# Performance work log

Measured on AMD Instinct MI355X. Metric: run time of the kernel, lower is better.

The kernel has to match this reference:

```python
import jax, jax.numpy as jnp
import numpy as np
from jax import lax

# Static config (matches init_kwargs)
DIM = 256; DR = 4; GROUP = 2; NH = 4; KS = 3; NA = 1; NUM_CLASS = 80; MUL = 5.0
CR = DIM // DR            # reduced dim = 64
GC = CR // GROUP          # offset-group channels = 32
HC = CR // NH             # per-head dim = 16
SCALE = HC ** -0.5
B, H, W = 8, 64, 64


def setup_inputs() -> dict:
    key = jax.random.key(0)
    ks_ = jax.random.split(key, 8)
    x = jax.random.normal(ks_[0], (B, DIM, H, W), jnp.float32)
    # offset = absolute pixel coordinates of the base sampling grid
    offset = jax.random.uniform(ks_[1], (B, NA * 2 * KS * KS, H, W), jnp.float32) * (H - 1)
    return dict(
        x=x, offset=offset,
        ln1_g=jnp.ones((DIM,), jnp.float32), ln1_b=jnp.zeros((DIM,), jnp.float32),
        w_qkv=jax.random.normal(ks_[2], (3 * CR, DIM), jnp.float32) * 0.02,
        w_dw=jax.random.normal(ks_[3], (GC, 1, 3, 3), jnp.float32) * 0.1,
        ln2_g=jnp.ones((GC,), jnp.float32), ln2_b=jnp.zeros((GC,), jnp.float32),
        w_off=jax.random.normal(ks_[4], (NA * 2 * KS * KS, GC, 3, 3), jnp.float32) * 0.02,
        b_off=jnp.zeros((NA * 2 * KS * KS,), jnp.float32),
        rpb_table=jax.random.normal(ks_[5], (1, NH, 1, 1, KS * KS, HC), jnp.float32) * 0.02,
        w_proj=jax.random.normal(ks_[6], (DIM, CR), jnp.float32) * 0.02,
        b_proj=jnp.zeros((DIM,), jnp.float32),
        w_cls=jax.random.normal(ks_[7], (NUM_CLASS, DIM), jnp.float32) * 0.02,
        b_cls=jnp.zeros((NUM_CLASS,), jnp.float32),
    )


def _ln_chw(x, g, b, eps=1e-5):
    # LayerNorm over channel dim of NCHW tensor (LayerNormProxy)
    xt = jnp.moveaxis(x, 1, -1)
    m = xt.mean(-1, keepdims=True)
    v = ((xt - m) ** 2).mean(-1, keepdims=True)
    y = (xt - m) * lax.rsqrt(v + eps) * g + b
    return jnp.moveaxis(y, -1, 1)


def _conv(x, w, groups=1, pad=1):
    return lax.conv_general_dilated(x, w, (1, 1), [(pad, pad), (pad, pad)],
                                    feature_group_count=groups,
                                    dimension_numbers=('NCHW', 'OIHW', 'NCHW'))


def _grid_sample(img, grid):
    # img [N,C,H,W]; grid [N,Ho,Wo,2] with (x,y) in [-1,1]; bilinear, zeros pad, align_corners=True
    N, C, Hi, Wi = img.shape
    gx = (grid[..., 0] + 1.0) * 0.5 * (Wi - 1)
    gy = (grid[..., 1] + 1.0) * 0.5 * (Hi - 1)
    x0 = jnp.floor(gx); y0 = jnp.floor(gy)
    x1 = x0 + 1.0;      y1 = y0 + 1.0

    def gather(ix, iy):
        valid = (ix >= 0) & (ix <= Wi - 1) & (iy >= 0) & (iy <= Hi - 1)
        ixc = jnp.clip(ix, 0, Wi - 1).astype(jnp.int32)
        iyc = jnp.clip(iy, 0, Hi - 1).astype(jnp.int32)
        v = jax.vmap(lambda im, yy, xx: im[:, yy, xx])(img, iyc, ixc)  # [N,C,Ho,Wo]
        return v * valid[:, None].astype(img.dtype)

    wa = ((x1 - gx) * (y1 - gy))[:, None]
    wb = ((gx - x0) * (y1 - gy))[:, None]
    wc = ((x1 - gx) * (gy - y0))[:, None]
    wd = ((gx - x0) * (gy - y0))[:, None]
    return (gather(x0, y0) * wa + gather(x1, y0) * wb +
            gather(x0, y1) * wc + gather(x1, y1) * wd)


def _extract_feats(feat, off, Hh, Ww):
    # feat [Bg,GC,H,W]; off [Bg, NA*2*KS*KS, H, W] in pixel coords (row, col)
    Bg = feat.shape[0]
    o = off.reshape(Bg, NA, KS, KS, 2, Hh, Ww)
    o = o.transpose(0, 1, 2, 5, 3, 6, 4)                  # b na kh h kw w d
    o = o.reshape(Bg, NA * KS * Hh, KS * Ww, 2)
    gy = 2.0 * o[..., 0] / (Hh - 1) - 1.0                  # row coord
    gx = 2.0 * o[..., 1] / (Ww - 1) - 1.0                  # col coord
    grid = jnp.stack([gx, gy], -1)                         # flip(-1): (x, y)
    out = _grid_sample(feat, grid)                         # [Bg,GC,NA*KS*H,KS*W]
    out = out.reshape(Bg, GC, NA, KS, Hh, KS, Ww)
    out = out.transpose(0, 2, 3, 5, 1, 4, 6).reshape(Bg, NA * KS * KS, GC, Hh, Ww)
    return out


def reference(x, offset, ln1_g, ln1_b, w_qkv, w_dw, ln2_g, ln2_b, w_off, b_off,
              rpb_table, w_proj, b_proj, w_cls, b_cls):
    Bb, C, Hh, Ww = x.shape
    N = KS * KS

    x_ = _ln_chw(x, ln1_g, ln1_b)
    qkv = jnp.einsum('oc,bchw->bohw', w_qkv, x_)           # [B,3*CR,H,W]
    q, k, v = jnp.split(qkv, 3, axis=1)                    # each [B,CR,H,W]

    # --- offset prediction ---
    q_off = q.reshape(Bb * GROUP, GC, Hh, Ww)
    t = _conv(q_off, w_dw, groups=GC)                      # depthwise 3x3
    t = _ln_chw(t, ln2_g, ln2_b)
    t = jax.nn.gelu(t, approximate=False)
    pred_offset = _conv(t, w_off) + b_off[None, :, None, None]

    off = jnp.broadcast_to(offset[:, None], (Bb, GROUP, NA * 2 * N, Hh, Ww))
    off = off.reshape(Bb * GROUP, NA * 2 * N, Hh, Ww)
    off = jnp.tanh(pred_offset) * MUL + off

    # --- deformable gather of k/v ---
    k = _extract_feats(k.reshape(Bb * GROUP, GC, Hh, Ww), off, Hh, Ww)
    v = _extract_feats(v.reshape(Bb * GROUP, GC, Hh, Ww), off, Hh, Ww)

    def to_heads(t):
        # [(b g), na*n, gc, h, w] -> [b, nh, hw, na, n, hc]
        t = t.reshape(Bb, GROUP, NA, N, GC, Hh, Ww)
        t = t.transpose(0, 5, 6, 2, 3, 1, 4)               # b h w na n g gc
        t = t.reshape(Bb, Hh * Ww, NA, N, NH, HC)
        return t.transpose(0, 4, 1, 2, 3, 5)

    k = to_heads(k) + rpb_table                            # [B,NH,HW,NA,N,HC]
    v = to_heads(v)

    q = q.reshape(Bb, NH, HC, Hh * Ww).transpose(0, 1, 3, 2)  # [B,NH,HW,HC]
    q = jnp.broadcast_to((q * SCALE)[:, :, :, None, :], (Bb, NH, Hh * Ww, NA, HC))

    attn = jnp.einsum('bnpac,bnpakc->bnpak', q, k)         # [B,NH,HW,NA,N]
    attn = jax.nn.softmax(attn, axis=-1)
    out = jnp.einsum('bnpak,bnpakc->bnpac', attn, v)       # [B,NH,HW,NA,HC]

    out = out.transpose(0, 2, 3, 1, 4).reshape(Bb, Hh * Ww, NA, CR)
    out = out @ w_proj.T + b_proj                          # [B,HW,NA,C]
    out = out + x.transpose(0, 2, 3, 1).reshape(Bb, Hh * Ww, 1, C)

    cls = out @ w_cls.T + b_cls                            # [B,HW,NA,NUM_CLASS]
    cls = cls.reshape(Bb, Hh, Ww, NA, NUM_CLASS).transpose(0, 3, 4, 1, 2)
    return cls.reshape(Bb, NA * NUM_CLASS, Hh, Ww)
```

## Files before the change

### kernel.cpp

```cpp
#include <hip/hip_runtime.h>
#include <hip/hip_fp16.h>
#include <math.h>

#define BB   8
#define HW   4096
#define BHW  32768
#define DIM  256
#define CR   64
#define GC   32
#define NHD  4
#define HC   16
#define NTAP 9
#define NCLS 80

#define OFF_QP   0u
#define OFF_QT   2097152u
#define OFF_KT   4194304u
#define OFF_T    8388608u
#define OFF_WBF  8388608u
#define OFF_AB   8437760u
#define OFF_OFFB 10485760u
#define OFF_AOT  11665408u
#define OFF_WPT  13762560u
#define OFF_WCT  13778944u
#define OFF_WFT  13799424u

typedef short bf16x8 __attribute__((ext_vector_type(8)));
typedef float f32x4  __attribute__((ext_vector_type(4)));

__device__ __forceinline__ unsigned short f2bf(float f) {
    unsigned u = __float_as_uint(f);
    unsigned r = u + 0x7FFFu + ((u >> 16) & 1u);
    return (unsigned short)(r >> 16);
}

__global__ __launch_bounds__(256) void k0_prep(
    const float* __restrict__ wqkv, const float* __restrict__ g1,
    const float* __restrict__ b1, const float* __restrict__ woff,
    const float* __restrict__ wproj, const float* __restrict__ wcls,
    float* __restrict__ ws)
{
    const int t = threadIdx.x;
    const int blk = blockIdx.x;
    if (blk < 192) {
        const int o = blk;
        unsigned short* wbf = (unsigned short*)(ws + OFF_WBF);
        wbf[o * 256 + t] = f2bf(wqkv[o * 256 + t] * g1[t]);
    } else if (blk < 448) {
        const int r = blk - 192;
        unsigned short* wpb = (unsigned short*)(ws + OFF_WPT);
        unsigned short* wcb = (unsigned short*)(ws + OFF_WCT);
        if (t < 64) wpb[r * 64 + t] = f2bf(wproj[r * 64 + t]);
        if (r < 80) wcb[r * 256 + t] = f2bf(wcls[r * 256 + t]);
    } else {
        if (t < 192) {
            float a = 0.f, bb = 0.f;
            for (int c = 0; c < 256; ++c) {
                float w = wqkv[t * 256 + c];
                a += w * g1[c]; bb += w * b1[c];
            }
            ws[OFF_AB + t] = a;
            ws[OFF_AB + 192 + t] = bb;
            for (int pair = t; pair < 288; pair += 192) {
                int wo = pair >> 5, ic = pair & 31;
                for (int o = 0; o < 18; ++o)
                    ws[OFF_WFT + (wo * 32 + ic) * 18 + o] = woff[(o * 32 + ic) * 9 + wo];
            }
        }
    }
}

__global__ __launch_bounds__(512) void k1_mfma(
    const float* __restrict__ x, float* __restrict__ ws)
{
    __shared__ float tile[64 * 193];
    const int t = threadIdx.x;
    const int b = blockIdx.x & 7, row = blockIdx.x >> 3;
    const int wv = __builtin_amdgcn_readfirstlane(t >> 6);
    const int pt = wv & 3, oh = wv >> 2;
    const int lane = t & 63;
    const int quad = lane >> 4, pxl = lane & 15;
    const int colbase = row * 64 + pt * 16 + pxl;
    const unsigned short* wbf = (const unsigned short*)(ws + OFF_WBF);
    const float* AB = ws + OFF_AB;

    f32x4 acc[6];
    #pragma unroll
    for (int ot = 0; ot < 6; ++ot) acc[ot] = (f32x4){0.f, 0.f, 0.f, 0.f};
    float s = 0.f, ss = 0.f;
    const size_t xb0 = (size_t)b * DIM * HW + colbase;

    for (int ks = 0; ks < 8; ++ks) {
        const int cbase = ks * 32 + quad * 8;
        float xv[8];
        #pragma unroll
        for (int j = 0; j < 8; ++j) {
            xv[j] = x[xb0 + (size_t)(cbase + j) * HW];
            s += xv[j]; ss += xv[j] * xv[j];
        }
        union { bf16x8 v; unsigned short u[8]; } bfrag;
        #pragma unroll
        for (int j = 0; j < 8; ++j) bfrag.u[j] = f2bf(xv[j]);
        #pragma unroll
        for (int ot = 0; ot < 6; ++ot) {
            const int orow = (oh * 6 + ot) * 16 + pxl;
            union { float4 f; bf16x8 v; } afrag;
            afrag.f = *(const float4*)&wbf[orow * 256 + cbase];
            acc[ot] = __builtin_amdgcn_mfma_f32_16x16x32_bf16(afrag.v, bfrag.v, acc[ot], 0, 0, 0);
        }
    }

    s  += __shfl_xor(s, 16, 64);  s  += __shfl_xor(s, 32, 64);
    ss += __shfl_xor(ss, 16, 64); ss += __shfl_xor(ss, 32, 64);
    const float m = s * (1.f / 256.f);
    const float rsv = rsqrtf(ss * (1.f / 256.f) - m * m + 1e-5f);

    const int px = pt * 16 + pxl;
    #pragma unroll
    for (int ot = 0; ot < 6; ++ot) {
        #pragma unroll
        for (int r = 0; r < 4; ++r) {
            int o = (oh * 6 + ot) * 16 + quad * 4 + r;
            tile[px * 193 + o] = rsv * (acc[ot][r] - m * AB[o]) + AB[192 + o];
        }
    }
    __syncthreads();

    float*  qp  = ws + OFF_QP;
    __half* qth = (__half*)(ws + OFF_QT);
    __half* kvh = (__half*)(ws + OFF_KT);
    const int colrow = row * 64;
    #pragma unroll
    for (int it = 0; it < 8; ++it) {
        int idx = it * 512 + t;
        int o = idx >> 6, px2 = idx & 63;
        qp[(size_t)(b * 64 + o) * HW + colrow + px2] = tile[px2 * 193 + o];
    }
    #pragma unroll
    for (int it = 0; it < 8; ++it) {
        int idx = it * 512 + t;
        int px2 = idx >> 6, o = idx & 63;
        qth[(size_t)(b * HW + colrow + px2) * 64 + o] = __float2half(tile[px2 * 193 + o]);
    }
    #pragma unroll
    for (int it = 0; it < 4; ++it) {
        int idx = it * 512 + t;
        int px2 = idx >> 5, ch32 = idx & 31;
        int sB = ch32 >> 4, ch = ch32 & 15;
        kvh[(size_t)((2 * b) * HW + colrow + px2) * 64 + sB * 32 + ch]
            = __float2half(tile[px2 * 193 + 64 + ch32]);
    }
    #pragma unroll
    for (int it = 0; it < 4; ++it) {
        int idx = it * 512 + t;
        int px2 = idx >> 5, ch32 = idx & 31;
        int sB = ch32 >> 4, ch = ch32 & 15;
        kvh[(size_t)((2 * b + 1) * HW + colrow + px2) * 64 + sB * 32 + ch]
            = __float2half(tile[px2 * 193 + 96 + ch32]);
    }
    #pragma unroll
    for (int it = 0; it < 4; ++it) {
        int idx = it * 512 + t;
        int px2 = idx >> 5, ch32 = idx & 31;
        int sB = ch32 >> 4, ch = ch32 & 15;
        kvh[(size_t)((2 * b) * HW + colrow + px2) * 64 + sB * 32 + 16 + ch]
            = __float2half(tile[px2 * 193 + 128 + ch32]);
    }
    #pragma unroll
    for (int it = 0; it < 4; ++it) {
        int idx = it * 512 + t;
        int px2 = idx >> 5, ch32 = idx & 31;
        int sB = ch32 >> 4, ch = ch32 & 15;
        kvh[(size_t)((2 * b + 1) * HW + colrow + px2) * 64 + sB * 32 + 16 + ch]
            = __float2half(tile[px2 * 193 + 160 + ch32]);
    }
}

__global__ __launch_bounds__(256) void k2_off_feat(
    const float* __restrict__ wdw, const float* __restrict__ g2, const float* __restrict__ b2,
    float* __restrict__ ws)
{
    __shared__ float qtile[3][32][64];
    __shared__ float rsum[4][64], rsq[4][64], smv[64], srv[64];
    const int t = threadIdx.x;
    const int bg = blockIdx.x >> 6, row = blockIdx.x & 63;
    const int p = t & 63;
    const int cq = __builtin_amdgcn_readfirstlane(t >> 6);
    const int b = bg >> 1, g = bg & 1;
    const float* qp = ws + OFF_QP;

    #pragma unroll
    for (int it = 0; it < 6; ++it) {
        int idx = it * 256 + t;
        int rc = idx >> 4;
        int seg = (idx & 15) << 2;
        int dyy = rc >> 5, ch = rc & 31;
        int y = row + dyy - 1;
        float4 v = make_float4(0.f, 0.f, 0.f, 0.f);
        if ((unsigned)y < 64u)
            v = *(const float4*)&qp[(size_t)(b * 64 + g * 32 + ch) * HW + y * 64 + seg];
        *(float4*)&qtile[dyy][ch][seg] = v;
    }
    __syncthreads();

    float vals[8];
    float s = 0.f, ss = 0.f;
    #pragma unroll
    for (int i = 0; i < 8; ++i) {
        int ch = cq * 8 + i;
        float a = 0.f;
        #pragma unroll
        for (int dy = 0; dy < 3; ++dy) {
            #pragma unroll
            for (int dx = 0; dx < 3; ++dx) {
                int xx = p + dx - 1;
                bool vld = (unsigned)xx < 64u;
                float q = qtile[dy][ch][vld ? xx : 0];
                a += (vld ? q : 0.f) * wdw[ch * 9 + dy * 3 + dx];
            }
        }
        vals[i] = a; s += a; ss += a * a;
    }
    rsum[cq][p] = s; rsq[cq][p] = ss;
    __syncthreads();
    if (t < 64) {
        float S = rsum[0][t] + rsum[1][t] + rsum[2][t] + rsum[3][t];
        float Q = rsq[0][t] + rsq[1][t] + rsq[2][t] + rsq[3][t];
        float m = S * (1.f / 32.f);
        float v = Q * (1.f / 32.f) - m * m;
        smv[t] = m; srv[t] = rsqrtf(v + 1e-5f);
    }
    __syncthreads();
    float m = smv[p], rv = srv[p];
    float* tb = ws + OFF_T;
    #pragma unroll
    for (int i = 0; i < 8; ++i) {
        int ch = cq * 8 + i;
        float u = (vals[i] - m) * rv * g2[ch] + b2[ch];
        float ge = 0.5f * u * (1.f + erff(u * 0.70710678118654752f));
        tb[(size_t)(bg * 32 + ch) * HW + row * 64 + p] = ge;
    }
}

__global__ __launch_bounds__(256) void k3_pred_off(
    const float* __restrict__ boff, const float* __restrict__ off_in,
    float* __restrict__ ws)
{
    __shared__ float part[4 * 18 * 64];
    const int t = threadIdx.x;
    const int bg = blockIdx.x >> 6, row = blockIdx.x & 63;
    const int p = t & 63;
    const int icq = __builtin_amdgcn_readfirstlane(t >> 6);
    const int b = bg >> 1;
    const float* tb = ws + OFF_T;
    const float* wfT = ws + OFF_WFT;
    float acc[18];
    #pragma unroll
    for (int o = 0; o < 18; ++o) acc[o] = 0.f;
    #pragma unroll
    for (int dy = 0; dy < 3; ++dy) {
        int y = row + dy - 1;
        if ((unsigned)y >= 64u) continue;
        #pragma unroll
        for (int dx = 0; dx < 3; ++dx) {
            int xx = p + dx - 1;
            bool vld = (unsigned)xx < 64u;
            int xc = vld ? xx : 0;
            int wo = dy * 3 + dx;
            #pragma unroll
            for (int i = 0; i < 8; ++i) {
                int ic = icq * 8 + i;
                float tv = tb[(size_t)(bg * 32 + ic) * HW + y * 64 + xc];
                tv = vld ? tv : 0.f;
                const float* wrow = wfT + (wo * 32 + ic) * 18;
                #pragma unroll
                for (int o = 0; o < 18; ++o)
                    acc[o] += tv * wrow[o];
            }
        }
    }
    #pragma unroll
    for (int o = 0; o < 18; ++o) part[(icq * 18 + o) * 64 + p] = acc[o];
    __syncthreads();
    float* ob = ws + OFF_OFFB;
    #pragma unroll
    for (int r = 0; r < 5; ++r) {
        int idx = t + r * 256;
        if (idx < 1152) {
            int o = idx >> 6, p2 = idx & 63;
            float v = part[o * 64 + p2] + part[(18 + o) * 64 + p2]
                    + part[(36 + o) * 64 + p2] + part[(54 + o) * 64 + p2] + boff[o];
            v = tanhf(v) * 5.0f + off_in[(size_t)(b * 18 + o) * HW + row * 64 + p2];
            ob[(size_t)(bg * 18 + o) * HW + row * 64 + p2] = v;
        }
    }
}

__global__ __launch_bounds__(256, 2) void k4_attn(
    const float* __restrict__ rpb, float* __restrict__ ws)
{
    __shared__ float rpb_l[NHD * NTAP * HC];
    for (int i = threadIdx.x; i < NHD * NTAP * HC; i += 256) rpb_l[i] = rpb[i];
    __syncthreads();

    const int t = threadIdx.x;
    const int wave = __builtin_amdgcn_readfirstlane(t >> 6);
    const int g = wave & 1, pxh = wave >> 1;
    const int lane = t & 63;
    const int pxl = lane & 7;
    const int prt = lane >> 3;
    const int s    = prt >> 2;
    const int half = (prt >> 1) & 1;
    const int j    = prt & 1;
    const int b = blockIdx.x & 7;
    const int chunk = blockIdx.x >> 3;
    const int hw = chunk * 16 + pxh * 8 + pxl;
    const int pix = b * HW + hw;
    const int bg = b * 2 + g;
    const int head = g * 2 + s;

    const __half* qth = (const __half*)(ws + OFF_QT);
    const __half* kvh = (const __half*)(ws + OFF_KT);
    const float*  ob  = ws + OFF_OFFB;

    union F4H { float4 f; __half2 h[4]; };
    F4H qld;
    qld.f = *(const float4*)&qth[(size_t)pix * 64 + g * 32 + s * 16 + j * 8];
    const float qs = half ? 0.0f : 0.25f;
    float qv[8];
    #pragma unroll
    for (int i = 0; i < 4; ++i) {
        float2 q2 = __half22float2(qld.h[i]);
        qv[2 * i] = q2.x * qs; qv[2 * i + 1] = q2.y * qs;
    }

    const float4* rb4 = (const float4*)(rpb_l + head * (NTAP * HC) + j * 8);
    const __half* kvp = kvh + (size_t)(bg * HW) * 64 + prt * 8;

    __half2 av[NTAP][4];
    float logit[NTAP];

    #pragma unroll
    for (int n = 0; n < NTAP; ++n) {
        float r = ob[(size_t)(bg * 18 + 2 * n) * HW + hw];
        float c = ob[(size_t)(bg * 18 + 2 * n + 1) * HW + hw];
        float y0f = floorf(r), x0f = floorf(c);
        float fy = r - y0f, fx = c - x0f;
        int iy0 = (int)y0f, ix0 = (int)x0f;
        float wts[4] = { (1.f - fx) * (1.f - fy), fx * (1.f - fy),
                         (1.f - fx) * fy,         fx * fy };
        __half2 acc0 = __float2half2_rn(0.f), acc1 = acc0, acc2 = acc0, acc3 = acc0;
        #pragma unroll
        for (int corner = 0; corner < 4; ++corner) {
            int cxx = ix0 + (corner & 1);
            int cyy = iy0 + (corner >> 1);
            bool vld = ((unsigned)cxx < 64u) && ((unsigned)cyy < 64u);
            float w = vld ? wts[corner] : 0.f;
            int cxc = min(max(cxx, 0), 63);
            int cyc = min(max(cyy, 0), 63);
            F4H kv;
            kv.f = *(const float4*)&kvp[(size_t)(cyc * 64 + cxc) * 64];
            __half2 w2 = __float2half2_rn(w);
            acc0 = __hfma2(kv.h[0], w2, acc0);
            acc1 = __hfma2(kv.h[1], w2, acc1);
            acc2 = __hfma2(kv.h[2], w2, acc2);
            acc3 = __hfma2(kv.h[3], w2, acc3);
        }
        av[n][0] = acc0; av[n][1] = acc1; av[n][2] = acc2; av[n][3] = acc3;
        float4 r0 = rb4[n * 4], r1 = rb4[n * 4 + 1];
        float2 a0 = __half22float2(acc0), a1 = __half22float2(acc1);
        float2 a2 = __half22float2(acc2), a3 = __half22float2(acc3);
        float part = qv[0] * (a0.x + r0.x) + qv[1] * (a0.y + r0.y)
                   + qv[2] * (a1.x + r0.z) + qv[3] * (a1.y + r0.w)
                   + qv[4] * (a2.x + r1.x) + qv[5] * (a2.y + r1.y)
                   + qv[6] * (a3.x + r1.z) + qv[7] * (a3.y + r1.w);
        part += __shfl_xor(part, 8, 64);
        part += __shfl_xor(part, 16, 64);
        logit[n] = part;
    }

    float m = logit[0];
    #pragma unroll
    for (int n = 1; n < NTAP; ++n) m = fmaxf(m, logit[n]);
    float l = 0.f;
    #pragma unroll
    for (int n = 0; n < NTAP; ++n) { logit[n] = __expf(logit[n] - m); l += logit[n]; }
    const float inv = 1.f / l;

    __half2 o0 = __float2half2_rn(0.f), o1 = o0, o2 = o0, o3 = o0;
    #pragma unroll
    for (int n = 0; n < NTAP; ++n) {
        __half2 p2 = __float2half2_rn(logit[n]);
        o0 = __hfma2(av[n][0], p2, o0);
        o1 = __hfma2(av[n][1], p2, o1);
        o2 = __hfma2(av[n][2], p2, o2);
        o3 = __hfma2(av[n][3], p2, o3);
    }
    if (half) {
        unsigned short* aob = (unsigned short*)(ws + OFF_AOT);
        const int cb = head * 16 + j * 8;
        float2 f0 = __half22float2(o0), f1 = __half22float2(o1);
        float2 f2 = __half22float2(o2), f3 = __half22float2(o3);
        union { float4 f; unsigned short u[8]; } pk;
        pk.u[0] = f2bf(f0.x * inv); pk.u[1] = f2bf(f0.y * inv);
        pk.u[2] = f2bf(f1.x * inv); pk.u[3] = f2bf(f1.y * inv);
        pk.u[4] = f2bf(f2.x * inv); pk.u[5] = f2bf(f2.y * inv);
        pk.u[6] = f2bf(f3.x * inv); pk.u[7] = f2bf(f3.y * inv);
        *(float4*)&aob[(size_t)pix * 64 + cb] = pk.f;
    }
}

__global__ __launch_bounds__(256) void k5_mfma(
    const float* __restrict__ x, const float* __restrict__ bproj,
    const float* __restrict__ bcls, float* __restrict__ ws, float* __restrict__ out)
{
    __shared__ unsigned short tmp[64][264];
    const int t = threadIdx.x;
    const int b = blockIdx.x & 7, row = blockIdx.x >> 3;
    const int wv = __builtin_amdgcn_readfirstlane(t >> 6);
    const int lane = t & 63, quad = lane >> 4, pxl = lane & 15;
    const int px = wv * 16 + pxl;
    const int pixcol = row * 64 + px;
    const size_t pix = (size_t)b * HW + pixcol;
    const unsigned short* aob = (const unsigned short*)(ws + OFF_AOT);
    const unsigned short* wpb = (const unsigned short*)(ws + OFF_WPT);
    const unsigned short* wcb = (const unsigned short*)(ws + OFF_WCT);

    union FB { float4 f; bf16x8 v; };
    FB bf0, bf1;
    bf0.f = *(const float4*)&aob[pix * 64 + quad * 8];
    bf1.f = *(const float4*)&aob[pix * 64 + 32 + quad * 8];

    #pragma unroll 4
    for (int ot = 0; ot < 16; ++ot) {
        f32x4 acc = (f32x4){0.f, 0.f, 0.f, 0.f};
        FB a0, a1;
        const int om = ot * 16 + pxl;
        a0.f = *(const float4*)&wpb[om * 64 + quad * 8];
        a1.f = *(const float4*)&wpb[om * 64 + 32 + quad * 8];
        acc = __builtin_amdgcn_mfma_f32_16x16x32_bf16(a0.v, bf0.v, acc, 0, 0, 0);
        acc = __builtin_amdgcn_mfma_f32_16x16x32_bf16(a1.v, bf1.v, acc, 0, 0, 0);
        union { unsigned short u[4]; ushort2 s2[2]; } pk;
        #pragma unroll
        for (int r = 0; r < 4; ++r) {
            int o = ot * 16 + quad * 4 + r;
            float v = acc[r] + bproj[o] + x[(size_t)(b * DIM + o) * HW + pixcol];
            pk.u[r] = f2bf(v);
        }
        *(ushort4*)&tmp[px][ot * 16 + quad * 4] = *(ushort4*)pk.u;
    }
    __syncthreads();

    f32x4 acc2[5];
    #pragma unroll
    for (int oc = 0; oc < 5; ++oc) acc2[oc] = (f32x4){0.f, 0.f, 0.f, 0.f};
    #pragma unroll
    for (int kc = 0; kc < 8; ++kc) {
        FB bb;
        bb.f = *(const float4*)&tmp[px][kc * 32 + quad * 8];
        #pragma unroll
        for (int oc = 0; oc < 5; ++oc) {
            FB aa;
            aa.f = *(const float4*)&wcb[(oc * 16 + pxl) * 256 + kc * 32 + quad * 8];
            acc2[oc] = __builtin_amdgcn_mfma_f32_16x16x32_bf16(aa.v, bb.v, acc2[oc], 0, 0, 0);
        }
    }
    #pragma unroll
    for (int oc = 0; oc < 5; ++oc) {
        #pragma unroll
        for (int r = 0; r < 4; ++r) {
            int o = oc * 16 + quad * 4 + r;
            out[(size_t)(b * NCLS + o) * HW + pixcol] = acc2[oc][r] + bcls[o];
        }
    }
}

extern "C" void kernel_launch(void* const* d_in, const int* in_sizes, int n_in,
                              void* d_out, int out_size, void* d_ws, size_t ws_size,
                              hipStream_t stream)
{
    const float* x     = (const float*)d_in[0];
    const float* off   = (const float*)d_in[1];
    const float* g1    = (const float*)d_in[2];
    const float* b1    = (const float*)d_in[3];
    const float* wqkv  = (const float*)d_in[4];
    const float* wdw   = (const float*)d_in[5];
    const float* g2    = (const float*)d_in[6];
    const float* b2    = (const float*)d_in[7];
    const float* woff  = (const float*)d_in[8];
    const float* boff  = (const float*)d_in[9];
    const float* rpb   = (const float*)d_in[10];
    const float* wproj = (const float*)d_in[11];
    const float* bproj = (const float*)d_in[12];
    const float* wcls  = (const float*)d_in[13];
    const float* bcls  = (const float*)d_in[14];
    float* ws  = (float*)d_ws;
    float* out = (float*)d_out;

    hipLaunchKernelGGL(k0_prep,     dim3(449),  dim3(256), 0, stream, wqkv, g1, b1, woff, wproj, wcls, ws);
    hipLaunchKernelGGL(k1_mfma,     dim3(512),  dim3(512), 0, stream, x, ws);
    hipLaunchKernelGGL(k2_off_feat, dim3(1024), dim3(256), 0, stream, wdw, g2, b2, ws);
    hipLaunchKernelGGL(k3_pred_off, dim3(1024), dim3(256), 0, stream, boff, off, ws);
    hipLaunchKernelGGL(k4_attn,     dim3(2048), dim3(256), 0, stream, rpb, ws);
    hipLaunchKernelGGL(k5_mfma,     dim3(512),  dim3(256), 0, stream, x, bproj, bcls, ws, out);
}
```

Before: 245.0 us.

## Fuse depthwise-conv/LN/GELU with offset-prediction conv using row halo recompute

Merges the offset-feature kernel and the offset-prediction kernel into one. Each block loads five q rows into shared memory and recomputes the depthwise conv, LayerNorm and GELU for three rows, so the 3x3 offset conv reads from shared memory instead of a global intermediate buffer. This drops one launch and a global write/read of the feature tensor, at the cost of computing the first stage three times over and using more LDS per block. It also raises the k4_attn launch-bounds occupancy hint from 2 to 4 blocks.

```diff
diff --git a/kernel.cpp b/kernel.cpp
--- a/kernel.cpp
+++ b/kernel.cpp
@@ -176,12 +176,19 @@
     }
 }
 
-__global__ __launch_bounds__(256) void k2_off_feat(
+__global__ __launch_bounds__(256) void k23_fused(
     const float* __restrict__ wdw, const float* __restrict__ g2, const float* __restrict__ b2,
+    const float* __restrict__ boff, const float* __restrict__ off_in,
     float* __restrict__ ws)
 {
-    __shared__ float qtile[3][32][64];
-    __shared__ float rsum[4][64], rsq[4][64], smv[64], srv[64];
+    __shared__ float smem[5 * 32 * 64 + 3 * 32 * 64 + 4 * 64 + 4 * 64 + 64 + 64];
+    float* q5   = smem;
+    float* t3   = smem + 5 * 32 * 64;
+    float* rsum = smem + 8 * 32 * 64;
+    float* rsq  = rsum + 4 * 64;
+    float* smv  = rsq + 4 * 64;
+    float* srv  = smv + 64;
+
     const int t = threadIdx.x;
     const int bg = blockIdx.x >> 6, row = blockIdx.x & 63;
     const int p = t & 63;
@@ -190,77 +197,72 @@
     const float* qp = ws + OFF_QP;
 
     #pragma unroll
-    for (int it = 0; it < 6; ++it) {
+    for (int it = 0; it < 10; ++it) {
         int idx = it * 256 + t;
         int rc = idx >> 4;
         int seg = (idx & 15) << 2;
         int dyy = rc >> 5, ch = rc & 31;
-        int y = row + dyy - 1;
+        int y = row + dyy - 2;
         float4 v = make_float4(0.f, 0.f, 0.f, 0.f);
         if ((unsigned)y < 64u)
             v = *(const float4*)&qp[(size_t)(b * 64 + g * 32 + ch) * HW + y * 64 + seg];
-        *(float4*)&qtile[dyy][ch][seg] = v;
+        *(float4*)&q5[(dyy * 32 + ch) * 64 + seg] = v;
     }
     __syncthreads();
 
-    float vals[8];
-    float s = 0.f, ss = 0.f;
-    #pragma unroll
-    for (int i = 0; i < 8; ++i) {
-        int ch = cq * 8 + i;
-        float a = 0.f;
-        #pragma unroll
-        for (int dy = 0; dy < 3; ++dy) {
+    for (int rr = 0; rr < 3; ++rr) {
+        const int y = row + rr - 1;
+        const bool yv = ((unsigned)y < 64u);
+        float vals[8] = {0.f, 0.f, 0.f, 0.f, 0.f, 0.f, 0.f, 0.f};
+        float s = 0.f, ssq = 0.f;
+        if (yv) {
             #pragma unroll
-            for (int dx = 0; dx < 3; ++dx) {
-                int xx = p + dx - 1;
-                bool vld = (unsigned)xx < 64u;
-                float q = qtile[dy][ch][vld ? xx : 0];
-                a += (vld ? q : 0.f) * wdw[ch * 9 + dy * 3 + dx];
+            for (int i = 0; i < 8; ++i) {
+                int ch = cq * 8 + i;
+                float a = 0.f;
+                #pragma unroll
+                for (int dy = 0; dy < 3; ++dy) {
+                    #pragma unroll
+                    for (int dx = 0; dx < 3; ++dx) {
+                        int xx = p + dx - 1;
+                        bool vld = (unsigned)xx < 64u;
+                        float q = q5[((rr + dy) * 32 + ch) * 64 + (vld ? xx : 0)];
+                        a += (vld ? q : 0.f) * wdw[ch * 9 + dy * 3 + dx];
+                    }
+                }
+                vals[i] = a; s += a; ssq += a * a;
             }
         }
-        vals[i] = a; s += a; ss += a * a;
-    }
-    rsum[cq][p] = s; rsq[cq][p] = ss;
-    __syncthreads();
-    if (t < 64) {
-        float S = rsum[0][t] + rsum[1][t] + rsum[2][t] + rsum[3][t];
-        float Q = rsq[0][t] + rsq[1][t] + rsq[2][t] + rsq[3][t];
-        float m = S * (1.f / 32.f);
-        float v = Q * (1.f / 32.f) - m * m;
-        smv[t] = m; srv[t] = rsqrtf(v + 1e-5f);
-    }
-    __syncthreads();
-    float m = smv[p], rv = srv[p];
-    float* tb = ws + OFF_T;
-    #pragma unroll
-    for (int i = 0; i < 8; ++i) {
-        int ch = cq * 8 + i;
-        float u = (vals[i] - m) * rv * g2[ch] + b2[ch];
-        float ge = 0.5f * u * (1.f + erff(u * 0.70710678118654752f));
-        tb[(size_t)(bg * 32 + ch) * HW + row * 64 + p] = ge;
-    }
-}
-
-__global__ __launch_bounds__(256) void k3_pred_off(
-    const float* __restrict__ boff, const float* __restrict__ off_in,
-    float* __restrict__ ws)
-{
-    __shared__ float part[4 * 18 * 64];
-    const int t = threadIdx.x;
-    const int bg = blockIdx.x >> 6, row = blockIdx.x & 63;
-    const int p = t & 63;
-    const int icq = __builtin_amdgcn_readfirstlane(t >> 6);
-    const int b = bg >> 1;
-    const float* tb = ws + OFF_T;
+        rsum[cq * 64 + p] = s; rsq[cq * 64 + p] = ssq;
+        __syncthreads();
+        if (t < 64) {
+            float S = rsum[t] + rsum[64 + t] + rsum[128 + t] + rsum[192 + t];
+            float Q = rsq[t] + rsq[64 + t] + rsq[128 + t] + rsq[192 + t];
+            float m = S * (1.f / 32.f);
+            float v = Q * (1.f / 32.f) - m * m;
+            smv[t] = m; srv[t] = rsqrtf(v + 1e-5f);
+        }
+        __syncthreads();
+        const float m = smv[p], rv = srv[p];
+        #pragma unroll
+        for (int i = 0; i < 8; ++i) {
+            int ch = cq * 8 + i;
+            float ge = 0.f;
+            if (yv) {
+                float u = (vals[i] - m) * rv * g2[ch] + b2[ch];
+                ge = 0.5f * u * (1.f + erff(u * 0.70710678118654752f));
+            }
+            t3[(rr * 32 + ch) * 64 + p] = ge;
+        }
+        __syncthreads();
+    }
+
     const float* wfT = ws + OFF_WFT;
     float acc[18];
     #pragma unroll
     for (int o = 0; o < 18; ++o) acc[o] = 0.f;
     #pragma unroll
     for (int dy = 0; dy < 3; ++dy) {
-        int y = row + dy - 1;
-        if ((unsigned)y >= 64u) continue;
         #pragma unroll
         for (int dx = 0; dx < 3; ++dx) {
             int xx = p + dx - 1;
@@ -269,8 +271,8 @@
             int wo = dy * 3 + dx;
             #pragma unroll
             for (int i = 0; i < 8; ++i) {
-                int ic = icq * 8 + i;
-                float tv = tb[(size_t)(bg * 32 + ic) * HW + y * 64 + xc];
+                int ic = cq * 8 + i;
+                float tv = t3[(dy * 32 + ic) * 64 + xc];
                 tv = vld ? tv : 0.f;
                 const float* wrow = wfT + (wo * 32 + ic) * 18;
                 #pragma unroll
@@ -279,8 +281,9 @@
             }
         }
     }
-    #pragma unroll
-    for (int o = 0; o < 18; ++o) part[(icq * 18 + o) * 64 + p] = acc[o];
+    float* part = q5;
+    #pragma unroll
+    for (int o = 0; o < 18; ++o) part[(cq * 18 + o) * 64 + p] = acc[o];
     __syncthreads();
     float* ob = ws + OFF_OFFB;
     #pragma unroll
@@ -296,7 +299,7 @@
     }
 }
 
-__global__ __launch_bounds__(256, 2) void k4_attn(
+__global__ __launch_bounds__(256, 4) void k4_attn(
     const float* __restrict__ rpb, float* __restrict__ ws)
 {
     __shared__ float rpb_l[NHD * NTAP * HC];
@@ -497,10 +500,9 @@
     float* ws  = (float*)d_ws;
     float* out = (float*)d_out;
 
-    hipLaunchKernelGGL(k0_prep,     dim3(449),  dim3(256), 0, stream, wqkv, g1, b1, woff, wproj, wcls, ws);
-    hipLaunchKernelGGL(k1_mfma,     dim3(512),  dim3(512), 0, stream, x, ws);
-    hipLaunchKernelGGL(k2_off_feat, dim3(1024), dim3(256), 0, stream, wdw, g2, b2, ws);
-    hipLaunchKernelGGL(k3_pred_off, dim3(1024), dim3(256), 0, stream, boff, off, ws);
-    hipLaunchKernelGGL(k4_attn,     dim3(2048), dim3(256), 0, stream, rpb, ws);
-    hipLaunchKernelGGL(k5_mfma,     dim3(512),  dim3(256), 0, stream, x, bproj, bcls, ws, out);
-}
+    hipLaunchKernelGGL(k0_prep,   dim3(449),  dim3(256), 0, stream, wqkv, g1, b1, woff, wproj, wcls, ws);
+    hipLaunchKernelGGL(k1_mfma,   dim3(512),  dim3(512), 0, stream, x, ws);
+    hipLaunchKernelGGL(k23_fused, dim3(1024), dim3(256), 0, stream, wdw, g2, b2, boff, off, ws);
+    hipLaunchKernelGGL(k4_attn,   dim3(2048), dim3(256), 0, stream, rpb, ws);
+    hipLaunchKernelGGL(k5_mfma,   dim3(512),  dim3(256), 0, stream, x, bproj, bcls, ws, out);
+}
```

After: 260.2 us. 1.06x slower.
